# Optimization experiments

Measured on AMD Instinct MI355X. Metric: run time of the kernel, lower is better.

The kernel has to match this reference:

```python
import jax, jax.numpy as jnp
import numpy as np

B, C, C1, C2, H, W = 16, 64, 16, 64, 128, 128

def setup_inputs() -> dict:
    key = jax.random.key(0)
    ks = jax.random.split(key, 8)
    s1 = 1.0 / np.sqrt(C1)
    s2 = 1.0 / np.sqrt(C)
    return {
        "x": jax.random.normal(ks[0], (B, C, H, W), dtype=jnp.float32),
        "e": jax.random.normal(ks[1], (B, C1, H, W), dtype=jnp.float32),
        "W1": jax.random.uniform(ks[2], (C2, C1), jnp.float32, -s1, s1),
        "b1": jax.random.uniform(ks[3], (C2,), jnp.float32, -s1, s1),
        "W2": jax.random.uniform(ks[4], (C2, C), jnp.float32, -s2, s2),
        "b2": jax.random.uniform(ks[5], (C2,), jnp.float32, -s2, s2),
        "W3": jax.random.uniform(ks[6], (C2, C), jnp.float32, -s2, s2),
        "b3": jax.random.uniform(ks[7], (C2,), jnp.float32, -s2, s2),
    }

def _conv1x1(inp, Wm, bv):
    # (B,Cin,H,W) x (Cout,Cin) -> (B,Cout,H,W)
    return jnp.einsum('bchw,oc->bohw', inp, Wm) + bv[None, :, None, None]

def reference(x, e, W1, b1, W2, b2, W3, b3):
    Bn, _, Hn, Wn = x.shape
    Q = _conv1x1(e, W1, b1).reshape(-1, Hn, Wn)   # (B*C2, H, W)
    V = _conv1x1(x, W2, b2).reshape(-1, Hn, Wn)
    K = _conv1x1(x, W3, b3).reshape(-1, Hn, Wn)
    score = jnp.einsum('nhw,ngw->nhg', Q, V)      # (B*C2, H, H), no scaling
    attn = jax.nn.softmax(score, axis=-1)
    ctx = jnp.einsum('nhg,ngw->nhw', attn, K)     # (B*C2, H, W)
    return ctx.reshape(Bn, -1, Hn, Wn)
```

## Files before the change

kernel.cpp:

```cpp
#include <hip/hip_runtime.h>

typedef __bf16 bf16_t;
typedef __bf16 bf16x8 __attribute__((ext_vector_type(8)));
typedef float f32x4 __attribute__((ext_vector_type(4)));

#define HW 16384
#define LOG2E 1.44269504088896f

__device__ __forceinline__ bf16_t f2b(float f) {
  unsigned u = __builtin_bit_cast(unsigned, f);
  u += 0x7fff + ((u >> 16) & 1);
  unsigned short s = (unsigned short)(u >> 16);
  return __builtin_bit_cast(bf16_t, s);
}

__global__ __launch_bounds__(256) void qvk_kernel(
    const float* __restrict__ x, const float* __restrict__ e,
    const float* __restrict__ W1, const float* __restrict__ b1,
    const float* __restrict__ W2, const float* __restrict__ b2,
    const float* __restrict__ W3, const float* __restrict__ b3,
    bf16_t* __restrict__ Qg, bf16_t* __restrict__ Vg, bf16_t* __restrict__ Kg)
{
  __shared__ bf16_t lx[256 * 64];
  __shared__ bf16_t le[256 * 32];
  __shared__ bf16_t rep[4][16 * 64];

  const int t = threadIdx.x;
  const int lane = t & 63;
  const int wv = t >> 6;
  const int b = blockIdx.x >> 6;
  const int p0 = (blockIdx.x & 63) << 8;

  {
    const int cq = (t >> 6) << 3;
    for (int half = 0; half < 2; ++half) {
      const int cc = cq + half * 32;
      for (int pp = 0; pp < 4; ++pp) {
        const int pl = pp * 64 + (t & 63);
        const float* src = x + (size_t)(b * 64 + cc) * HW + p0 + pl;
        bf16x8 v;
#pragma unroll
        for (int i = 0; i < 8; ++i) v[i] = f2b(src[(size_t)i * HW]);
        int byte = pl * 128 + cc * 2;
        byte ^= (pl & 7) << 4;
        *reinterpret_cast<bf16x8*>(reinterpret_cast<char*>(lx) + byte) = v;
      }
    }
  }
  {
    const int cq = (t & 3) << 3;
    const int pb = t >> 2;
    for (int pp = 0; pp < 4; ++pp) {
      const int pl = pp * 64 + pb;
      bf16x8 v;
#pragma unroll
      for (int i = 0; i < 8; ++i) {
        const int c = cq + i;
        float f = (c < 16) ? e[(size_t)(b * 16 + c) * HW + p0 + pl] : 0.0f;
        v[i] = f2b(f);
      }
      *reinterpret_cast<bf16x8*>(reinterpret_cast<char*>(le) + pl * 64 + cq * 2) = v;
    }
  }
  __syncthreads();

  const int pw0 = wv << 6;
  const int lr = lane & 15;
  const int lg = lane >> 4;
  const int kq = lg << 3;

  f32x4 acc[4][4];

  auto ldx = [&](int row, int c) -> bf16x8 {
    int byte = row * 128 + c * 2;
    byte ^= (row & 7) << 4;
    return *reinterpret_cast<const bf16x8*>(reinterpret_cast<const char*>(lx) + byte);
  };

  auto store_target = [&](const float* bias, bf16_t* G) {
    const int r0 = lg << 2;
#pragma unroll
    for (int mt = 0; mt < 4; ++mt) {
      float bv[4];
#pragma unroll
      for (int r = 0; r < 4; ++r) bv[r] = bias[mt * 16 + r0 + r];
#pragma unroll
      for (int nt = 0; nt < 4; ++nt)
#pragma unroll
        for (int r = 0; r < 4; ++r)
          rep[wv][(r0 + r) * 64 + nt * 16 + lr] = f2b(acc[mt][nt][r] + bv[r]);
      asm volatile("s_waitcnt lgkmcnt(0)" ::: "memory");
#pragma unroll
      for (int half = 0; half < 2; ++half) {
        const int row = half * 8 + (lane >> 3);
        const int colb = (lane & 7) << 3;
        bf16x8 v = *reinterpret_cast<const bf16x8*>(
            reinterpret_cast<const char*>(rep[wv]) + row * 128 + colb * 2);
        *reinterpret_cast<bf16x8*>(G + (size_t)(b * 64 + mt * 16 + row) * HW + p0 + pw0 + colb) = v;
      }
      asm volatile("s_waitcnt lgkmcnt(0)" ::: "memory");
    }
  };

#pragma unroll
  for (int mt = 0; mt < 4; ++mt)
#pragma unroll
    for (int nt = 0; nt < 4; ++nt) acc[mt][nt] = f32x4{0.f, 0.f, 0.f, 0.f};
#pragma unroll
  for (int kt = 0; kt < 2; ++kt) {
    bf16x8 A[4], Bf[4];
#pragma unroll
    for (int mt = 0; mt < 4; ++mt) {
      const float* wp = W2 + (size_t)(mt * 16 + lr) * 64 + kt * 32 + kq;
      bf16x8 a;
#pragma unroll
      for (int i = 0; i < 8; ++i) a[i] = f2b(wp[i]);
      A[mt] = a;
    }
#pragma unroll
    for (int nt = 0; nt < 4; ++nt) Bf[nt] = ldx(pw0 + nt * 16 + lr, kt * 32 + kq);
#pragma unroll
    for (int mt = 0; mt < 4; ++mt)
#pragma unroll
      for (int nt = 0; nt < 4; ++nt)
        acc[mt][nt] = __builtin_amdgcn_mfma_f32_16x16x32_bf16(A[mt], Bf[nt], acc[mt][nt], 0, 0, 0);
  }
  store_target(b2, Vg);

#pragma unroll
  for (int mt = 0; mt < 4; ++mt)
#pragma unroll
    for (int nt = 0; nt < 4; ++nt) acc[mt][nt] = f32x4{0.f, 0.f, 0.f, 0.f};
#pragma unroll
  for (int kt = 0; kt < 2; ++kt) {
    bf16x8 A[4], Bf[4];
#pragma unroll
    for (int mt = 0; mt < 4; ++mt) {
      const float* wp = W3 + (size_t)(mt * 16 + lr) * 64 + kt * 32 + kq;
      bf16x8 a;
#pragma unroll
      for (int i = 0; i < 8; ++i) a[i] = f2b(wp[i]);
      A[mt] = a;
    }
#pragma unroll
    for (int nt = 0; nt < 4; ++nt) Bf[nt] = ldx(pw0 + nt * 16 + lr, kt * 32 + kq);
#pragma unroll
    for (int mt = 0; mt < 4; ++mt)
#pragma unroll
      for (int nt = 0; nt < 4; ++nt)
        acc[mt][nt] = __builtin_amdgcn_mfma_f32_16x16x32_bf16(A[mt], Bf[nt], acc[mt][nt], 0, 0, 0);
  }
  store_target(b3, Kg);

#pragma unroll
  for (int mt = 0; mt < 4; ++mt)
#pragma unroll
    for (int nt = 0; nt < 4; ++nt) acc[mt][nt] = f32x4{0.f, 0.f, 0.f, 0.f};
  {
    bf16x8 A[4], Bf[4];
#pragma unroll
    for (int mt = 0; mt < 4; ++mt) {
      bf16x8 a;
      if (kq < 16) {
        const float* wp = W1 + (size_t)(mt * 16 + lr) * 16 + kq;
#pragma unroll
        for (int i = 0; i < 8; ++i) a[i] = f2b(wp[i]);
      } else {
#pragma unroll
        for (int i = 0; i < 8; ++i) a[i] = f2b(0.0f);
      }
      A[mt] = a;
    }
#pragma unroll
    for (int nt = 0; nt < 4; ++nt)
      Bf[nt] = *reinterpret_cast<const bf16x8*>(
          reinterpret_cast<const char*>(le) + (pw0 + nt * 16 + lr) * 64 + kq * 2);
#pragma unroll
    for (int mt = 0; mt < 4; ++mt)
#pragma unroll
      for (int nt = 0; nt < 4; ++nt)
        acc[mt][nt] = __builtin_amdgcn_mfma_f32_16x16x32_bf16(A[mt], Bf[nt], acc[mt][nt], 0, 0, 0);
  }
  store_target(b1, Qg);
}

__global__ __launch_bounds__(256) void attn_kernel(
    const bf16_t* __restrict__ Qg, const bf16_t* __restrict__ Vg,
    const bf16_t* __restrict__ Kg, float* __restrict__ out)
{
  __shared__ bf16_t bufA[128 * 128];
  __shared__ bf16_t bufB[128 * 128];

  const int n = blockIdx.x;
  const int t = threadIdx.x;
  const int lane = t & 63;
  const int wv = t >> 6;
  const int lr = lane & 15;
  const int lg = lane >> 4;
  const int kq = lg << 3;

  const bf16_t* Qn = Qg + (size_t)n * HW;
  const bf16_t* Vn = Vg + (size_t)n * HW;
  const bf16_t* Kn = Kg + (size_t)n * HW;

  for (int it = 0; it < 8; ++it) {
    const int chunk = it * 256 + t;
    const int row = chunk >> 4;
    int byte = (row << 8) + ((chunk & 15) << 4);
    byte ^= (row & 7) << 4;
    *reinterpret_cast<bf16x8*>(reinterpret_cast<char*>(bufA) + byte) =
        *reinterpret_cast<const bf16x8*>(Qn + chunk * 8);
    *reinterpret_cast<bf16x8*>(reinterpret_cast<char*>(bufB) + byte) =
        *reinterpret_cast<const bf16x8*>(Vn + chunk * 8);
  }
  __syncthreads();

  auto ldfrag = [&](const bf16_t* buf, int row, int c) -> bf16x8 {
    int byte = (row << 8) + (c << 1);
    byte ^= (row & 7) << 4;
    return *reinterpret_cast<const bf16x8*>(reinterpret_cast<const char*>(buf) + byte);
  };

  const int h0 = wv << 5;
  f32x4 acc[2][8];
#pragma unroll
  for (int mt = 0; mt < 2; ++mt)
#pragma unroll
    for (int nt = 0; nt < 8; ++nt) acc[mt][nt] = f32x4{0.f, 0.f, 0.f, 0.f};

#pragma unroll
  for (int kt = 0; kt < 4; ++kt) {
    bf16x8 A0 = ldfrag(bufA, h0 + lr,      kt * 32 + kq);
    bf16x8 A1 = ldfrag(bufA, h0 + 16 + lr, kt * 32 + kq);
#pragma unroll
    for (int nt = 0; nt < 8; ++nt) {
      bf16x8 Bv = ldfrag(bufB, nt * 16 + lr, kt * 32 + kq);
      acc[0][nt] = __builtin_amdgcn_mfma_f32_16x16x32_bf16(A0, Bv, acc[0][nt], 0, 0, 0);
      acc[1][nt] = __builtin_amdgcn_mfma_f32_16x16x32_bf16(A1, Bv, acc[1][nt], 0, 0, 0);
    }
  }

  float zrow[2][4];
#pragma unroll
  for (int mt = 0; mt < 2; ++mt) {
#pragma unroll
    for (int r = 0; r < 4; ++r) {
      float m = acc[mt][0][r];
#pragma unroll
      for (int nt = 1; nt < 8; ++nt) m = fmaxf(m, acc[mt][nt][r]);
      m = fmaxf(m, __shfl_xor(m, 1));
      m = fmaxf(m, __shfl_xor(m, 2));
      m = fmaxf(m, __shfl_xor(m, 4));
      m = fmaxf(m, __shfl_xor(m, 8));
      float z = 0.f;
#pragma unroll
      for (int nt = 0; nt < 8; ++nt) {
        float p = exp2f((acc[mt][nt][r] - m) * LOG2E);
        acc[mt][nt][r] = p;
        z += p;
      }
      z += __shfl_xor(z, 1);
      z += __shfl_xor(z, 2);
      z += __shfl_xor(z, 4);
      z += __shfl_xor(z, 8);
      zrow[mt][r] = z;
    }
  }
  __syncthreads();

#pragma unroll
  for (int mt = 0; mt < 2; ++mt) {
    const int rbase = h0 + mt * 16 + (lg << 2);
#pragma unroll
    for (int nt = 0; nt < 8; ++nt) {
#pragma unroll
      for (int r = 0; r < 4; ++r) {
        const int row = rbase + r;
        int byte = (row << 8) + ((nt * 16 + lr) << 1);
        byte ^= (row & 7) << 4;
        *reinterpret_cast<bf16_t*>(reinterpret_cast<char*>(bufB) + byte) = f2b(acc[mt][nt][r]);
      }
    }
  }
  for (int it = 0; it < 8; ++it) {
    const int w = t & 127;
    const int g0 = ((it << 1) + (t >> 7)) << 3;
    bf16x8 v;
#pragma unroll
    for (int i = 0; i < 8; ++i) v[i] = Kn[(g0 + i) * 128 + w];
    int byte = (w << 8) + (g0 << 1);
    byte ^= (w & 7) << 4;
    *reinterpret_cast<bf16x8*>(reinterpret_cast<char*>(bufA) + byte) = v;
  }
  __syncthreads();

  f32x4 acc2[2][8];
#pragma unroll
  for (int mt = 0; mt < 2; ++mt)
#pragma unroll
    for (int wt = 0; wt < 8; ++wt) acc2[mt][wt] = f32x4{0.f, 0.f, 0.f, 0.f};
#pragma unroll
  for (int kt = 0; kt < 4; ++kt) {
    bf16x8 A0 = ldfrag(bufB, h0 + lr,      kt * 32 + kq);
    bf16x8 A1 = ldfrag(bufB, h0 + 16 + lr, kt * 32 + kq);
#pragma unroll
    for (int wt = 0; wt < 8; ++wt) {
      bf16x8 Bk = ldfrag(bufA, wt * 16 + lr, kt * 32 + kq);
      acc2[0][wt] = __builtin_amdgcn_mfma_f32_16x16x32_bf16(A0, Bk, acc2[0][wt], 0, 0, 0);
      acc2[1][wt] = __builtin_amdgcn_mfma_f32_16x16x32_bf16(A1, Bk, acc2[1][wt], 0, 0, 0);
    }
  }

  float* On = out + (size_t)n * HW;
#pragma unroll
  for (int mt = 0; mt < 2; ++mt) {
    const int rbase = h0 + mt * 16 + (lg << 2);
#pragma unroll
    for (int r = 0; r < 4; ++r) {
      const float inv = 1.0f / zrow[mt][r];
#pragma unroll
      for (int wt = 0; wt < 8; ++wt)
        On[(rbase + r) * 128 + wt * 16 + lr] = acc2[mt][wt][r] * inv;
    }
  }
}

extern "C" void kernel_launch(void* const* d_in, const int* in_sizes, int n_in,
                              void* d_out, int out_size, void* d_ws, size_t ws_size,
                              hipStream_t stream) {
  const float* x  = (const float*)d_in[0];
  const float* e  = (const float*)d_in[1];
  const float* W1 = (const float*)d_in[2];
  const float* b1 = (const float*)d_in[3];
  const float* W2 = (const float*)d_in[4];
  const float* b2 = (const float*)d_in[5];
  const float* W3 = (const float*)d_in[6];
  const float* b3 = (const float*)d_in[7];
  float* out = (float*)d_out;

  bf16_t* Qg = (bf16_t*)d_ws;
  bf16_t* Vg = Qg + (size_t)1024 * HW;
  bf16_t* Kg = Vg + (size_t)1024 * HW;

  qvk_kernel<<<1024, 256, 0, stream>>>(x, e, W1, b1, W2, b2, W3, b3, Qg, Vg, Kg);
  attn_kernel<<<1024, 256, 0, stream>>>(Qg, Vg, Kg, out);
}
```

Measured before the change: 212.5 us.

## Swap MFMA operand roles to store results directly, preload Q into registers

In the projection kernel the MFMA operands are swapped so each lane holds four consecutive pixels of one output channel. Results are then written straight to global memory as packed 4×bf16 stores, removing the LDS staging buffer and its waits. In the attention kernel Q fragments are loaded directly into registers, K is transposed into LDS up front alongside V, and the second GEMM is computed transposed. That lets output rows be written as float4 vectors using a shared-memory table of reciprocal row sums. Launch-bounds occupancy hints and loop unrolling are also added, at the cost of narrower 8-byte global stores and extra register pressure.

```diff
diff --git a/kernel.cpp b/kernel.cpp
--- a/kernel.cpp
+++ b/kernel.cpp
@@ -3,6 +3,7 @@
 typedef __bf16 bf16_t;
 typedef __bf16 bf16x8 __attribute__((ext_vector_type(8)));
 typedef float f32x4 __attribute__((ext_vector_type(4)));
+typedef unsigned short u16x4_t __attribute__((ext_vector_type(4)));
 
 #define HW 16384
 #define LOG2E 1.44269504088896f
@@ -13,8 +14,11 @@
   unsigned short s = (unsigned short)(u >> 16);
   return __builtin_bit_cast(bf16_t, s);
 }
-
-__global__ __launch_bounds__(256) void qvk_kernel(
+__device__ __forceinline__ unsigned short b2u(bf16_t b) {
+  return __builtin_bit_cast(unsigned short, b);
+}
+
+__global__ __launch_bounds__(256, 3) void qvk_kernel(
     const float* __restrict__ x, const float* __restrict__ e,
     const float* __restrict__ W1, const float* __restrict__ b1,
     const float* __restrict__ W2, const float* __restrict__ b2,
@@ -23,7 +27,6 @@
 {
   __shared__ bf16_t lx[256 * 64];
   __shared__ bf16_t le[256 * 32];
-  __shared__ bf16_t rep[4][16 * 64];
 
   const int t = threadIdx.x;
   const int lane = t & 63;
@@ -32,11 +35,13 @@
   const int p0 = (blockIdx.x & 63) << 8;
 
   {
-    const int cq = (t >> 6) << 3;
+    const int cq = wv << 3;
+#pragma unroll
     for (int half = 0; half < 2; ++half) {
       const int cc = cq + half * 32;
+#pragma unroll
       for (int pp = 0; pp < 4; ++pp) {
-        const int pl = pp * 64 + (t & 63);
+        const int pl = pp * 64 + lane;
         const float* src = x + (size_t)(b * 64 + cc) * HW + p0 + pl;
         bf16x8 v;
 #pragma unroll
@@ -50,6 +55,7 @@
   {
     const int cq = (t & 3) << 3;
     const int pb = t >> 2;
+#pragma unroll
     for (int pp = 0; pp < 4; ++pp) {
       const int pl = pp * 64 + pb;
       bf16x8 v;
@@ -68,8 +74,6 @@
   const int lr = lane & 15;
   const int lg = lane >> 4;
   const int kq = lg << 3;
-
-  f32x4 acc[4][4];
 
   auto ldx = [&](int row, int c) -> bf16x8 {
     int byte = row * 128 + c * 2;
@@ -77,119 +81,104 @@
     return *reinterpret_cast<const bf16x8*>(reinterpret_cast<const char*>(lx) + byte);
   };
 
-  auto store_target = [&](const float* bias, bf16_t* G) {
-    const int r0 = lg << 2;
-#pragma unroll
-    for (int mt = 0; mt < 4; ++mt) {
-      float bv[4];
-#pragma unroll
-      for (int r = 0; r < 4; ++r) bv[r] = bias[mt * 16 + r0 + r];
-#pragma unroll
-      for (int nt = 0; nt < 4; ++nt)
-#pragma unroll
-        for (int r = 0; r < 4; ++r)
-          rep[wv][(r0 + r) * 64 + nt * 16 + lr] = f2b(acc[mt][nt][r] + bv[r]);
-      asm volatile("s_waitcnt lgkmcnt(0)" ::: "memory");
-#pragma unroll
-      for (int half = 0; half < 2; ++half) {
-        const int row = half * 8 + (lane >> 3);
-        const int colb = (lane & 7) << 3;
-        bf16x8 v = *reinterpret_cast<const bf16x8*>(
-            reinterpret_cast<const char*>(rep[wv]) + row * 128 + colb * 2);
-        *reinterpret_cast<bf16x8*>(G + (size_t)(b * 64 + mt * 16 + row) * HW + p0 + pw0 + colb) = v;
-      }
-      asm volatile("s_waitcnt lgkmcnt(0)" ::: "memory");
-    }
+  f32x4 acc[4][4];
+
+  auto do_xtarget = [&](const float* __restrict__ Wm, const float* __restrict__ bias,
+                        bf16_t* __restrict__ G) {
+#pragma unroll
+    for (int mt = 0; mt < 4; ++mt)
+#pragma unroll
+      for (int nt = 0; nt < 4; ++nt) acc[mt][nt] = f32x4{0.f, 0.f, 0.f, 0.f};
+#pragma unroll
+    for (int kt = 0; kt < 2; ++kt) {
+      bf16x8 Bw[4], Af[4];
+#pragma unroll
+      for (int nt = 0; nt < 4; ++nt) {
+        const float* wp = Wm + (size_t)(nt * 16 + lr) * 64 + kt * 32 + kq;
+        bf16x8 a;
+#pragma unroll
+        for (int i = 0; i < 8; ++i) a[i] = f2b(wp[i]);
+        Bw[nt] = a;
+      }
+#pragma unroll
+      for (int mt = 0; mt < 4; ++mt) Af[mt] = ldx(pw0 + mt * 16 + lr, kt * 32 + kq);
+#pragma unroll
+      for (int mt = 0; mt < 4; ++mt)
+#pragma unroll
+        for (int nt = 0; nt < 4; ++nt)
+          acc[mt][nt] = __builtin_amdgcn_mfma_f32_16x16x32_bf16(Af[mt], Bw[nt], acc[mt][nt], 0, 0, 0);
+    }
+    float bvv[4];
+#pragma unroll
+    for (int nt = 0; nt < 4; ++nt) bvv[nt] = bias[nt * 16 + lr];
+#pragma unroll
+    for (int nt = 0; nt < 4; ++nt)
+#pragma unroll
+      for (int mt = 0; mt < 4; ++mt) {
+        u16x4_t pk;
+#pragma unroll
+        for (int r = 0; r < 4; ++r) pk[r] = b2u(f2b(acc[mt][nt][r] + bvv[nt]));
+        *reinterpret_cast<u16x4_t*>(G + (size_t)(b * 64 + nt * 16 + lr) * HW
+                                      + p0 + pw0 + mt * 16 + (lg << 2)) = pk;
+      }
   };
 
-#pragma unroll
-  for (int mt = 0; mt < 4; ++mt)
-#pragma unroll
-    for (int nt = 0; nt < 4; ++nt) acc[mt][nt] = f32x4{0.f, 0.f, 0.f, 0.f};
-#pragma unroll
-  for (int kt = 0; kt < 2; ++kt) {
-    bf16x8 A[4], Bf[4];
-#pragma unroll
-    for (int mt = 0; mt < 4; ++mt) {
-      const float* wp = W2 + (size_t)(mt * 16 + lr) * 64 + kt * 32 + kq;
-      bf16x8 a;
-#pragma unroll
-      for (int i = 0; i < 8; ++i) a[i] = f2b(wp[i]);
-      A[mt] = a;
-    }
-#pragma unroll
-    for (int nt = 0; nt < 4; ++nt) Bf[nt] = ldx(pw0 + nt * 16 + lr, kt * 32 + kq);
-#pragma unroll
-    for (int mt = 0; mt < 4; ++mt)
-#pragma unroll
-      for (int nt = 0; nt < 4; ++nt)
-        acc[mt][nt] = __builtin_amdgcn_mfma_f32_16x16x32_bf16(A[mt], Bf[nt], acc[mt][nt], 0, 0, 0);
-  }
-  store_target(b2, Vg);
-
-#pragma unroll
-  for (int mt = 0; mt < 4; ++mt)
-#pragma unroll
-    for (int nt = 0; nt < 4; ++nt) acc[mt][nt] = f32x4{0.f, 0.f, 0.f, 0.f};
-#pragma unroll
-  for (int kt = 0; kt < 2; ++kt) {
-    bf16x8 A[4], Bf[4];
-#pragma unroll
-    for (int mt = 0; mt < 4; ++mt) {
-      const float* wp = W3 + (size_t)(mt * 16 + lr) * 64 + kt * 32 + kq;
-      bf16x8 a;
-#pragma unroll
-      for (int i = 0; i < 8; ++i) a[i] = f2b(wp[i]);
-      A[mt] = a;
-    }
-#pragma unroll
-    for (int nt = 0; nt < 4; ++nt) Bf[nt] = ldx(pw0 + nt * 16 + lr, kt * 32 + kq);
-#pragma unroll
-    for (int mt = 0; mt < 4; ++mt)
-#pragma unroll
-      for (int nt = 0; nt < 4; ++nt)
-        acc[mt][nt] = __builtin_amdgcn_mfma_f32_16x16x32_bf16(A[mt], Bf[nt], acc[mt][nt], 0, 0, 0);
-  }
-  store_target(b3, Kg);
+  do_xtarget(W2, b2, Vg);
+  do_xtarget(W3, b3, Kg);
 
 #pragma unroll
   for (int mt = 0; mt < 4; ++mt)
 #pragma unroll
     for (int nt = 0; nt < 4; ++nt) acc[mt][nt] = f32x4{0.f, 0.f, 0.f, 0.f};
   {
-    bf16x8 A[4], Bf[4];
-#pragma unroll
-    for (int mt = 0; mt < 4; ++mt) {
+    bf16x8 Bw[4], Af[4];
+#pragma unroll
+    for (int nt = 0; nt < 4; ++nt) {
       bf16x8 a;
       if (kq < 16) {
-        const float* wp = W1 + (size_t)(mt * 16 + lr) * 16 + kq;
+        const float* wp = W1 + (size_t)(nt * 16 + lr) * 16 + kq;
 #pragma unroll
         for (int i = 0; i < 8; ++i) a[i] = f2b(wp[i]);
       } else {
 #pragma unroll
         for (int i = 0; i < 8; ++i) a[i] = f2b(0.0f);
       }
-      A[mt] = a;
-    }
+      Bw[nt] = a;
+    }
+#pragma unroll
+    for (int mt = 0; mt < 4; ++mt)
+      Af[mt] = *reinterpret_cast<const bf16x8*>(
+          reinterpret_cast<const char*>(le) + (pw0 + mt * 16 + lr) * 64 + kq * 2);
+#pragma unroll
+    for (int mt = 0; mt < 4; ++mt)
+#pragma unroll
+      for (int nt = 0; nt < 4; ++nt)
+        acc[mt][nt] = __builtin_amdgcn_mfma_f32_16x16x32_bf16(Af[mt], Bw[nt], acc[mt][nt], 0, 0, 0);
+  }
+  {
+    float bvv[4];
+#pragma unroll
+    for (int nt = 0; nt < 4; ++nt) bvv[nt] = b1[nt * 16 + lr];
 #pragma unroll
     for (int nt = 0; nt < 4; ++nt)
-      Bf[nt] = *reinterpret_cast<const bf16x8*>(
-          reinterpret_cast<const char*>(le) + (pw0 + nt * 16 + lr) * 64 + kq * 2);
-#pragma unroll
-    for (int mt = 0; mt < 4; ++mt)
-#pragma unroll
-      for (int nt = 0; nt < 4; ++nt)
-        acc[mt][nt] = __builtin_amdgcn_mfma_f32_16x16x32_bf16(A[mt], Bf[nt], acc[mt][nt], 0, 0, 0);
-  }
-  store_target(b1, Qg);
-}
-
-__global__ __launch_bounds__(256) void attn_kernel(
+#pragma unroll
+      for (int mt = 0; mt < 4; ++mt) {
+        u16x4_t pk;
+#pragma unroll
+        for (int r = 0; r < 4; ++r) pk[r] = b2u(f2b(acc[mt][nt][r] + bvv[nt]));
+        *reinterpret_cast<u16x4_t*>(Qg + (size_t)(b * 64 + nt * 16 + lr) * HW
+                                      + p0 + pw0 + mt * 16 + (lg << 2)) = pk;
+      }
+  }
+}
+
+__global__ __launch_bounds__(256, 2) void attn_kernel(
     const bf16_t* __restrict__ Qg, const bf16_t* __restrict__ Vg,
     const bf16_t* __restrict__ Kg, float* __restrict__ out)
 {
-  __shared__ bf16_t bufA[128 * 128];
-  __shared__ bf16_t bufB[128 * 128];
+  __shared__ bf16_t bufK[128 * 128];
+  __shared__ bf16_t bufV[128 * 128];
+  __shared__ float zl[128];
 
   const int n = blockIdx.x;
   const int t = threadIdx.x;
@@ -198,20 +187,39 @@
   const int lr = lane & 15;
   const int lg = lane >> 4;
   const int kq = lg << 3;
+  const int h0 = wv << 5;
 
   const bf16_t* Qn = Qg + (size_t)n * HW;
   const bf16_t* Vn = Vg + (size_t)n * HW;
   const bf16_t* Kn = Kg + (size_t)n * HW;
 
+  bf16x8 qf[4][2];
+#pragma unroll
+  for (int kt = 0; kt < 4; ++kt)
+#pragma unroll
+    for (int mt = 0; mt < 2; ++mt)
+      qf[kt][mt] = *reinterpret_cast<const bf16x8*>(
+          Qn + (h0 + mt * 16 + lr) * 128 + kt * 32 + kq);
+
+#pragma unroll
   for (int it = 0; it < 8; ++it) {
     const int chunk = it * 256 + t;
     const int row = chunk >> 4;
     int byte = (row << 8) + ((chunk & 15) << 4);
     byte ^= (row & 7) << 4;
-    *reinterpret_cast<bf16x8*>(reinterpret_cast<char*>(bufA) + byte) =
-        *reinterpret_cast<const bf16x8*>(Qn + chunk * 8);
-    *reinterpret_cast<bf16x8*>(reinterpret_cast<char*>(bufB) + byte) =
+    *reinterpret_cast<bf16x8*>(reinterpret_cast<char*>(bufV) + byte) =
         *reinterpret_cast<const bf16x8*>(Vn + chunk * 8);
+  }
+#pragma unroll
+  for (int it = 0; it < 8; ++it) {
+    const int w = t & 127;
+    const int g0 = ((it << 1) + (t >> 7)) << 3;
+    bf16x8 v;
+#pragma unroll
+    for (int i = 0; i < 8; ++i) v[i] = Kn[(g0 + i) * 128 + w];
+    int byte = (w << 8) + (g0 << 1);
+    byte ^= (w & 7) << 4;
+    *reinterpret_cast<bf16x8*>(reinterpret_cast<char*>(bufK) + byte) = v;
   }
   __syncthreads();
 
@@ -221,22 +229,18 @@
     return *reinterpret_cast<const bf16x8*>(reinterpret_cast<const char*>(buf) + byte);
   };
 
-  const int h0 = wv << 5;
   f32x4 acc[2][8];
 #pragma unroll
   for (int mt = 0; mt < 2; ++mt)
 #pragma unroll
     for (int nt = 0; nt < 8; ++nt) acc[mt][nt] = f32x4{0.f, 0.f, 0.f, 0.f};
-
 #pragma unroll
   for (int kt = 0; kt < 4; ++kt) {
-    bf16x8 A0 = ldfrag(bufA, h0 + lr,      kt * 32 + kq);
-    bf16x8 A1 = ldfrag(bufA, h0 + 16 + lr, kt * 32 + kq);
 #pragma unroll
     for (int nt = 0; nt < 8; ++nt) {
-      bf16x8 Bv = ldfrag(bufB, nt * 16 + lr, kt * 32 + kq);
-      acc[0][nt] = __builtin_amdgcn_mfma_f32_16x16x32_bf16(A0, Bv, acc[0][nt], 0, 0, 0);
-      acc[1][nt] = __builtin_amdgcn_mfma_f32_16x16x32_bf16(A1, Bv, acc[1][nt], 0, 0, 0);
+      bf16x8 Bv = ldfrag(bufV, nt * 16 + lr, kt * 32 + kq);
+      acc[0][nt] = __builtin_amdgcn_mfma_f32_16x16x32_bf16(qf[kt][0], Bv, acc[0][nt], 0, 0, 0);
+      acc[1][nt] = __builtin_amdgcn_mfma_f32_16x16x32_bf16(qf[kt][1], Bv, acc[1][nt], 0, 0, 0);
     }
   }
 
@@ -271,6 +275,10 @@
 #pragma unroll
   for (int mt = 0; mt < 2; ++mt) {
     const int rbase = h0 + mt * 16 + (lg << 2);
+    if (lr == 0) {
+#pragma unroll
+      for (int r = 0; r < 4; ++r) zl[rbase + r] = 1.0f / zrow[mt][r];
+    }
 #pragma unroll
     for (int nt = 0; nt < 8; ++nt) {
 #pragma unroll
@@ -278,19 +286,9 @@
         const int row = rbase + r;
         int byte = (row << 8) + ((nt * 16 + lr) << 1);
         byte ^= (row & 7) << 4;
-        *reinterpret_cast<bf16_t*>(reinterpret_cast<char*>(bufB) + byte) = f2b(acc[mt][nt][r]);
-      }
-    }
-  }
-  for (int it = 0; it < 8; ++it) {
-    const int w = t & 127;
-    const int g0 = ((it << 1) + (t >> 7)) << 3;
-    bf16x8 v;
-#pragma unroll
-    for (int i = 0; i < 8; ++i) v[i] = Kn[(g0 + i) * 128 + w];
-    int byte = (w << 8) + (g0 << 1);
-    byte ^= (w & 7) << 4;
-    *reinterpret_cast<bf16x8*>(reinterpret_cast<char*>(bufA) + byte) = v;
+        *reinterpret_cast<bf16_t*>(reinterpret_cast<char*>(bufV) + byte) = f2b(acc[mt][nt][r]);
+      }
+    }
   }
   __syncthreads();
 
@@ -298,29 +296,30 @@
 #pragma unroll
   for (int mt = 0; mt < 2; ++mt)
 #pragma unroll
-    for (int wt = 0; wt < 8; ++wt) acc2[mt][wt] = f32x4{0.f, 0.f, 0.f, 0.f};
+    for (int nt = 0; nt < 8; ++nt) acc2[mt][nt] = f32x4{0.f, 0.f, 0.f, 0.f};
 #pragma unroll
   for (int kt = 0; kt < 4; ++kt) {
-    bf16x8 A0 = ldfrag(bufB, h0 + lr,      kt * 32 + kq);
-    bf16x8 A1 = ldfrag(bufB, h0 + 16 + lr, kt * 32 + kq);
-#pragma unroll
-    for (int wt = 0; wt < 8; ++wt) {
-      bf16x8 Bk = ldfrag(bufA, wt * 16 + lr, kt * 32 + kq);
-      acc2[0][wt] = __builtin_amdgcn_mfma_f32_16x16x32_bf16(A0, Bk, acc2[0][wt], 0, 0, 0);
-      acc2[1][wt] = __builtin_amdgcn_mfma_f32_16x16x32_bf16(A1, Bk, acc2[1][wt], 0, 0, 0);
+    bf16x8 A0 = ldfrag(bufK, h0 + lr,      kt * 32 + kq);
+    bf16x8 A1 = ldfrag(bufK, h0 + 16 + lr, kt * 32 + kq);
+#pragma unroll
+    for (int nt = 0; nt < 8; ++nt) {
+      bf16x8 Bp = ldfrag(bufV, nt * 16 + lr, kt * 32 + kq);
+      acc2[0][nt] = __builtin_amdgcn_mfma_f32_16x16x32_bf16(A0, Bp, acc2[0][nt], 0, 0, 0);
+      acc2[1][nt] = __builtin_amdgcn_mfma_f32_16x16x32_bf16(A1, Bp, acc2[1][nt], 0, 0, 0);
     }
   }
 
   float* On = out + (size_t)n * HW;
 #pragma unroll
-  for (int mt = 0; mt < 2; ++mt) {
-    const int rbase = h0 + mt * 16 + (lg << 2);
-#pragma unroll
-    for (int r = 0; r < 4; ++r) {
-      const float inv = 1.0f / zrow[mt][r];
-#pragma unroll
-      for (int wt = 0; wt < 8; ++wt)
-        On[(rbase + r) * 128 + wt * 16 + lr] = acc2[mt][wt][r] * inv;
+  for (int nt = 0; nt < 8; ++nt) {
+    const float zv = zl[nt * 16 + lr];
+#pragma unroll
+    for (int mt = 0; mt < 2; ++mt) {
+      f32x4 o;
+#pragma unroll
+      for (int r = 0; r < 4; ++r) o[r] = acc2[mt][nt][r] * zv;
+      *reinterpret_cast<f32x4*>(On + (size_t)(nt * 16 + lr) * 128
+                                + h0 + mt * 16 + (lg << 2)) = o;
     }
   }
 }
```

Measured after the change: 215.9 us. No clear change (+1.6%).
